# Optimization experiments

Measured on AMD Instinct MI355X. Metric: run time of the kernel, lower is better.

## Reference

```python
import jax, jax.numpy as jnp
import numpy as np

N = 50000      # nodes
E = 600000     # edges (avg degree 12)
F_IN = 64      # raw node features
HID = 128      # hidden_size
HEADS = 8
DH = HID // HEADS  # 16, per-head dim = out_channels
C = 10         # classes
L = 3          # num_gnn_layers


def setup_inputs() -> dict:
    key = jax.random.key(0)
    ks = jax.random.split(key, 12)
    g = lambda k, shape, fan: jax.random.normal(k, shape, jnp.float32) / np.float32(np.sqrt(fan))
    return {
        "x": jax.random.normal(ks[0], (N, F_IN), jnp.float32),
        "edge_index": jax.random.randint(ks[1], (2, E), 0, N, dtype=jnp.int32),
        "distance": jax.random.uniform(ks[2], (E, 1), jnp.float32),
        "Wq": g(ks[3], (L, HID, HID), HID), "bq": jnp.zeros((L, HID), jnp.float32),
        "Wk": g(ks[4], (L, HID, HID), HID), "bk": jnp.zeros((L, HID), jnp.float32),
        "Wv": g(ks[5], (L, HID, HID), HID), "bv": jnp.zeros((L, HID), jnp.float32),
        "We": g(ks[6], (L, 1, HID), 1),
        "Ws": g(ks[7], (L, HID, HID), HID), "bs": jnp.zeros((L, HID), jnp.float32),
        "ln_g": jnp.ones((L, HID), jnp.float32), "ln_b": jnp.zeros((L, HID), jnp.float32),
        "W_before": g(ks[8], (F_IN, HID), F_IN), "b_before": jnp.zeros((HID,), jnp.float32),
        "W_after": g(ks[9], (HID, C), HID), "b_after": jnp.zeros((C,), jnp.float32),
    }


def _layer_norm(h, gamma, beta):
    m = h.mean(-1, keepdims=True)
    v = ((h - m) ** 2).mean(-1, keepdims=True)
    return (h - m) * jax.lax.rsqrt(v + 1e-5) * gamma + beta


def _transformer_conv(h, src, dst, ea, Wq, bq, Wk, bk, Wv, bv, We, Ws, bs):
    # PyG TransformerConv (concat=True, beta=False, root_weight=True), eval mode (no dropout)
    q = (h @ Wq + bq).reshape(-1, HEADS, DH)   # [N,H,D]
    k = (h @ Wk + bk).reshape(-1, HEADS, DH)
    v = (h @ Wv + bv).reshape(-1, HEADS, DH)
    e = (ea @ We).reshape(-1, HEADS, DH)       # [E,H,D] edge embedding (no bias)
    ke = k[src] + e                            # gather keys along edges
    alpha = (q[dst] * ke).sum(-1) / np.float32(np.sqrt(DH))  # [E,H]
    # segment softmax over incoming edges per destination node
    amax = jax.ops.segment_max(alpha, dst, num_segments=N)
    amax = jnp.where(jnp.isfinite(amax), amax, 0.0)
    ex = jnp.exp(alpha - amax[dst])
    den = jax.ops.segment_sum(ex, dst, num_segments=N)
    a = ex / (den[dst] + 1e-16)                # [E,H]
    msg = (v[src] + e) * a[..., None]          # weighted values
    out = jax.ops.segment_sum(msg, dst, num_segments=N).reshape(-1, HEADS * DH)
    return out + h @ Ws + bs                   # root/skip connection


def reference(x, edge_index, distance, Wq, bq, Wk, bk, Wv, bv, We, Ws, bs,
              ln_g, ln_b, W_before, b_before, W_after, b_after):
    src, dst = edge_index[0], edge_index[1]
    h = jax.nn.relu(x @ W_before + b_before)   # fcnn_before
    for i in range(L):
        h = _transformer_conv(h, src, dst, distance,
                              Wq[i], bq[i], Wk[i], bk[i], Wv[i], bv[i],
                              We[i], Ws[i], bs[i])
        if i < L - 1:
            h = jax.nn.relu(_layer_norm(h, ln_g[i], ln_b[i]))
    # fcnn_after
    h = jax.nn.relu(_layer_norm(h, ln_g[L - 1], ln_b[L - 1]))
    h = h @ W_after + b_after
    return jax.nn.log_softmax(h, axis=1)
```

## Files before the change

kernel.cpp:

```cpp
#include <hip/hip_runtime.h>
#include <cstdint>
#include <cstddef>

#define NN 50000
#define NE 600000
#define FIN 64
#define HID 128
#define NCLS 10
#define NLAYER 3

#define QSCALE 0.36067376022224085f

typedef __bf16 bf16x8 __attribute__((ext_vector_type(8)));
typedef float f32x4 __attribute__((ext_vector_type(4)));
typedef float f32x2 __attribute__((ext_vector_type(2)));

__device__ __forceinline__ unsigned short f2bf(float f) {
    unsigned int u = __builtin_bit_cast(unsigned int, f);
    u += 0x7fffu + ((u >> 16) & 1u);
    return (unsigned short)(u >> 16);
}
__device__ __forceinline__ float bf2f(unsigned short s) {
    unsigned int u = ((unsigned int)s) << 16;
    return __builtin_bit_cast(float, u);
}

__global__ __launch_bounds__(256) void k_prep(
    const float* __restrict__ Wq, const float* __restrict__ Wk,
    const float* __restrict__ Wv, const float* __restrict__ Ws,
    const float* __restrict__ Wbe, const float* __restrict__ Waf,
    unsigned short* __restrict__ Wt12,
    unsigned short* __restrict__ Wbt,
    float* __restrict__ Wat,
    const int* __restrict__ edst, int* __restrict__ counts)
{
    int blk = blockIdx.x;
    int tid = threadIdx.x;
    if (blk < 768) {
        int m = blk >> 6;
        int l = m >> 2, which = m & 3;
        const float* src;
        if (which == 0) src = Wq; else if (which == 1) src = Wk;
        else if (which == 2) src = Wv; else src = Ws;
        src += (size_t)l * HID * HID;
        int idx = (blk & 63) * 256 + tid;
        int c = idx >> 7, k = idx & 127;
        Wt12[(size_t)m * 16384 + (size_t)c * 128 + k] = f2bf(src[(size_t)k * 128 + c]);
    } else if (blk < 800) {
        int idx = (blk - 768) * 256 + tid;
        int c = idx >> 6, k = idx & 63;
        Wbt[(size_t)c * 64 + k] = f2bf(Wbe[(size_t)k * 128 + c]);
    } else if (blk < 805) {
        int i = (blk - 800) * 256 + tid;
        if (i < 1280) {
            int c = i >> 7, f = i & 127;
            Wat[i] = Waf[f * 10 + c];
        }
    } else {
        int e = (blk - 805) * 256 + tid;
        if (e < NE) atomicAdd(&counts[edst[e]], 1);
    }
}

__global__ __launch_bounds__(512) void k_scan1(const int* __restrict__ counts,
                                               int* __restrict__ row_ptr,
                                               int* __restrict__ partials, int n) {
    __shared__ int sm[512];
    int tid = threadIdx.x;
    int i = blockIdx.x * 512 + tid;
    int v = (i < n) ? counts[i] : 0;
    sm[tid] = v;
    __syncthreads();
    #pragma unroll
    for (int off = 1; off < 512; off <<= 1) {
        int t = (tid >= off) ? sm[tid - off] : 0;
        __syncthreads();
        sm[tid] += t;
        __syncthreads();
    }
    if (i < n) row_ptr[i] = sm[tid] - v;
    if (tid == 511) partials[blockIdx.x] = sm[511];
}

__global__ __launch_bounds__(128) void k_scan2(int* __restrict__ partials, int nb) {
    __shared__ int sm[128];
    int t = threadIdx.x;
    int v = (t < nb) ? partials[t] : 0;
    sm[t] = v;
    __syncthreads();
    #pragma unroll
    for (int off = 1; off < 128; off <<= 1) {
        int x = (t >= off) ? sm[t - off] : 0;
        __syncthreads();
        sm[t] += x;
        __syncthreads();
    }
    if (t < nb) partials[t] = sm[t] - v;
}

__global__ __launch_bounds__(512) void k_scan3(int* __restrict__ row_ptr,
                                               const int* __restrict__ partials, int n) {
    int i = blockIdx.x * 512 + threadIdx.x;
    if (i < n) row_ptr[i] += partials[blockIdx.x];
}

__global__ __launch_bounds__(256) void k_fill(const int* __restrict__ esrc,
                                              const int* __restrict__ edst,
                                              const float* __restrict__ dist,
                                              int* __restrict__ cursor,
                                              const int* __restrict__ row_ptr,
                                              int2* __restrict__ srcd) {
    int e = blockIdx.x * 256 + threadIdx.x;
    if (e < NE) {
        int d = edst[e];
        int pos = atomicAdd(&cursor[d], 1);
        srcd[row_ptr[d] + pos] = make_int2(esrc[e], __float_as_int(dist[e]));
    }
}

__device__ __forceinline__ void qkvs_store(
    int m, int arow, int colb, f32x4 acc, float4 bb, int nrows,
    unsigned short* __restrict__ qb, unsigned char* __restrict__ kv8,
    unsigned short* __restrict__ hsb)
{
    if (arow >= nrows) return;
    float v0 = acc[0] + bb.x, v1 = acc[1] + bb.y;
    float v2 = acc[2] + bb.z, v3 = acc[3] + bb.w;
    if (m == 0) {
        ushort4 o;
        o.x = f2bf(v0 * QSCALE); o.y = f2bf(v1 * QSCALE);
        o.z = f2bf(v2 * QSCALE); o.w = f2bf(v3 * QSCALE);
        *(ushort4*)(qb + (size_t)arow * 128 + colb) = o;
    } else if (m == 1 || m == 2) {
        unsigned int pk = __builtin_amdgcn_cvt_pk_fp8_f32(v0, v1, 0, false);
        pk = __builtin_amdgcn_cvt_pk_fp8_f32(v2, v3, pk, true);
        *(unsigned int*)(kv8 + (size_t)arow * 256 + (colb >> 2) * 8 + (m == 2 ? 4 : 0)) = pk;
    } else {
        ushort4 o;
        o.x = f2bf(v0); o.y = f2bf(v1); o.z = f2bf(v2); o.w = f2bf(v3);
        *(ushort4*)(hsb + (size_t)arow * 128 + colb) = o;
    }
}

__global__ __launch_bounds__(512) void k_qkvs(
    const unsigned short* __restrict__ Ab, int nrows,
    const unsigned short* __restrict__ Wt,
    const float* __restrict__ bq, const float* __restrict__ bk,
    const float* __restrict__ bv, const float* __restrict__ bs,
    unsigned short* __restrict__ qb,
    unsigned char* __restrict__ kv8,
    unsigned short* __restrict__ hsb)
{
    const int tid = threadIdx.x;
    const int w = tid >> 6, lane = tid & 63;
    const int m = w >> 1, ch = w & 1;
    const float* bias = (m == 0) ? bq : (m == 1) ? bk : (m == 2) ? bv : bs;
    const unsigned short* Wm = Wt + (size_t)m * 16384;
    const int lc = lane & 15, lk = lane >> 4;

    bf16x8 bw[4][4];
    float4 bb[4];
    #pragma unroll
    for (int ct = 0; ct < 4; ++ct) {
        int col = ch * 64 + ct * 16 + lc;
        bb[ct] = *(const float4*)(bias + ch * 64 + ct * 16 + lk * 4);
        #pragma unroll
        for (int kb = 0; kb < 4; ++kb)
            bw[ct][kb] = *(const bf16x8*)(Wm + (size_t)col * 128 + kb * 32 + lk * 8);
    }

    const int r0 = blockIdx.x * 64;
    #pragma unroll
    for (int rt = 0; rt < 4; ++rt) {
        const int arow = r0 + rt * 16 + lc;
        const bool rv = arow < nrows;
        bf16x8 z = {};
        bf16x8 a[4];
        #pragma unroll
        for (int kb = 0; kb < 4; ++kb)
            a[kb] = rv ? *(const bf16x8*)(Ab + (size_t)arow * 128 + kb * 32 + lk * 8) : z;
        #pragma unroll
        for (int ct = 0; ct < 4; ++ct) {
            f32x4 acc = {0.f, 0.f, 0.f, 0.f};
            #pragma unroll
            for (int kb = 0; kb < 4; ++kb)
                acc = __builtin_amdgcn_mfma_f32_16x16x32_bf16(bw[ct][kb], a[kb], acc, 0, 0, 0);
            qkvs_store(m, arow, ch * 64 + ct * 16 + lk * 4, acc, bb[ct], nrows, qb, kv8, hsb);
        }
    }
}

__global__ __launch_bounds__(512) void k_gqkvs(
    const float* __restrict__ x, int nrows,
    const unsigned short* __restrict__ Wbt,
    const float* __restrict__ bbe,
    const unsigned short* __restrict__ Wt,
    const float* __restrict__ bq, const float* __restrict__ bk,
    const float* __restrict__ bv, const float* __restrict__ bs,
    unsigned short* __restrict__ qb,
    unsigned char* __restrict__ kv8,
    unsigned short* __restrict__ hsb)
{
    __shared__ unsigned short hs_s[64 * 136];
    const int tid = threadIdx.x;
    const int w = tid >> 6, lane = tid & 63;
    const int lc = lane & 15, lk = lane >> 4;
    const int r0 = blockIdx.x * 64;

    {
        const int rt0 = w & 3, ch0 = w >> 2;
        const int arl = rt0 * 16 + lc;
        const int arow = r0 + arl;
        const bool rv = arow < nrows;
        bf16x8 a[2];
        #pragma unroll
        for (int kb = 0; kb < 2; ++kb) {
            union { bf16x8 v; unsigned short u[8]; } t;
            #pragma unroll
            for (int q = 0; q < 2; ++q) {
                float4 f = rv ? *(const float4*)(x + (size_t)arow * 64 + kb * 32 + lk * 8 + q * 4)
                              : make_float4(0.f, 0.f, 0.f, 0.f);
                t.u[q * 4 + 0] = f2bf(f.x); t.u[q * 4 + 1] = f2bf(f.y);
                t.u[q * 4 + 2] = f2bf(f.z); t.u[q * 4 + 3] = f2bf(f.w);
            }
            a[kb] = t.v;
        }
        #pragma unroll
        for (int ct = 0; ct < 4; ++ct) {
            const int col = ch0 * 64 + ct * 16 + lc;
            f32x4 acc = {0.f, 0.f, 0.f, 0.f};
            #pragma unroll
            for (int kb = 0; kb < 2; ++kb) {
                bf16x8 bwf = *(const bf16x8*)(Wbt + (size_t)col * 64 + kb * 32 + lk * 8);
                acc = __builtin_amdgcn_mfma_f32_16x16x32_bf16(bwf, a[kb], acc, 0, 0, 0);
            }
            float4 bv_ = *(const float4*)(bbe + ch0 * 64 + ct * 16 + lk * 4);
            ushort4 o;
            o.x = rv ? f2bf(fmaxf(acc[0] + bv_.x, 0.f)) : 0;
            o.y = rv ? f2bf(fmaxf(acc[1] + bv_.y, 0.f)) : 0;
            o.z = rv ? f2bf(fmaxf(acc[2] + bv_.z, 0.f)) : 0;
            o.w = rv ? f2bf(fmaxf(acc[3] + bv_.w, 0.f)) : 0;
            *(ushort4*)(hs_s + arl * 136 + ch0 * 64 + ct * 16 + lk * 4) = o;
        }
    }
    __syncthreads();

    const int m = w >> 1, ch = w & 1;
    const float* bias = (m == 0) ? bq : (m == 1) ? bk : (m == 2) ? bv : bs;
    const unsigned short* Wm = Wt + (size_t)m * 16384;

    bf16x8 bw[4][4];
    float4 bb[4];
    #pragma unroll
    for (int ct = 0; ct < 4; ++ct) {
        int col = ch * 64 + ct * 16 + lc;
        bb[ct] = *(const float4*)(bias + ch * 64 + ct * 16 + lk * 4);
        #pragma unroll
        for (int kb = 0; kb < 4; ++kb)
            bw[ct][kb] = *(const bf16x8*)(Wm + (size_t)col * 128 + kb * 32 + lk * 8);
    }

    #pragma unroll
    for (int rt = 0; rt < 4; ++rt) {
        const int arl = rt * 16 + lc;
        const int arow = r0 + arl;
        bf16x8 a[4];
        #pragma unroll
        for (int kb = 0; kb < 4; ++kb)
            a[kb] = *(const bf16x8*)(hs_s + arl * 136 + kb * 32 + lk * 8);
        #pragma unroll
        for (int ct = 0; ct < 4; ++ct) {
            f32x4 acc = {0.f, 0.f, 0.f, 0.f};
            #pragma unroll
            for (int kb = 0; kb < 4; ++kb)
                acc = __builtin_amdgcn_mfma_f32_16x16x32_bf16(bw[ct][kb], a[kb], acc, 0, 0, 0);
            qkvs_store(m, arow, ch * 64 + ct * 16 + lk * 4, acc, bb[ct], nrows, qb, kv8, hsb);
        }
    }
}

#define FET(Ki, i) {                                                      \
    int e_ = base + 2 * (i) + half;                                       \
    int ec_ = e_ < cmax ? e_ : 0;                                         \
    int sx_ = __shfl(sd0.x, ec_);                                         \
    Ki = *(const uint2*)(kv8 + (size_t)sx_ * 256 + l5 * 8); }

#define CMP(Ki, i) {                                                      \
    int e_ = base + 2 * (i) + half;                                       \
    bool val_ = e_ < cmax;                                                \
    int ec_ = val_ ? e_ : 0;                                              \
    float dd_ = __int_as_float(__shfl(sd0.y, ec_));                       \
    f32x2 k01_ = __builtin_amdgcn_cvt_pk_f32_fp8(Ki.x, false);            \
    f32x2 k23_ = __builtin_amdgcn_cvt_pk_f32_fp8(Ki.x, true);             \
    float p_ = q0 * k01_.x + q1 * k01_.y + q2 * k23_.x + q3 * k23_.y;     \
    p_ += __shfl_xor(p_, 1);                                              \
    p_ += __shfl_xor(p_, 2);                                              \
    p_ = fmaf(dd_, qwe, p_);                                              \
    float w_ = val_ ? exp2f(p_) : 0.f;                                    \
    s += w_;                                                              \
    sd = fmaf(dd_, w_, sd);                                               \
    f32x2 v01_ = __builtin_amdgcn_cvt_pk_f32_fp8(Ki.y, false);            \
    f32x2 v23_ = __builtin_amdgcn_cvt_pk_f32_fp8(Ki.y, true);             \
    va0 = fmaf(v01_.x, w_, va0); va1 = fmaf(v01_.y, w_, va1);             \
    va2 = fmaf(v23_.x, w_, va2); va3 = fmaf(v23_.y, w_, va3); }

template <int LAST>
__global__ __launch_bounds__(256, 6) void k_attn(
    const unsigned short* __restrict__ qb,
    const unsigned short* __restrict__ hsb,
    const unsigned char* __restrict__ kv8,
    const int2* __restrict__ srcd,
    const float* __restrict__ We,
    const int* __restrict__ row_ptr,
    const float* __restrict__ lng,
    const float* __restrict__ lnb,
    unsigned short* __restrict__ hb,
    const float* __restrict__ Wat,
    const float* __restrict__ ba,
    float* __restrict__ out, int nnodes)
{
    const int wid = threadIdx.x >> 6;
    const int lane = threadIdx.x & 63;
    const int n = blockIdx.x * 4 + wid;
    if (n >= nnodes) return;
    const int half = lane >> 5;
    const int l5 = lane & 31;
    const int d0 = l5 * 4;

    const int beg = row_ptr[n];
    const int cnt = row_ptr[n + 1] - beg;

    ushort4 qu = *(const ushort4*)(qb + (size_t)n * 128 + d0);
    const float q0 = bf2f(qu.x), q1 = bf2f(qu.y), q2 = bf2f(qu.z), q3 = bf2f(qu.w);
    const float4 wv = *(const float4*)(We + d0);
    float qwe = q0 * wv.x + q1 * wv.y + q2 * wv.z + q3 * wv.w;
    qwe += __shfl_xor(qwe, 1);
    qwe += __shfl_xor(qwe, 2);

    float s = 0.f, sd = 0.f;
    float va0 = 0.f, va1 = 0.f, va2 = 0.f, va3 = 0.f;

    if (cnt > 0) {
        int2 sd0 = srcd[beg + (lane < cnt ? lane : 0)];
        const int cmax = cnt < 64 ? cnt : 64;
        const int nch = (cmax + 15) >> 4;
        for (int ch = 0; ch < nch; ++ch) {
            const int base = ch << 4;
            uint2 kA, kB, kC, kD, kE, kF, kG, kH;
            FET(kA, 0) FET(kB, 1) FET(kC, 2) FET(kD, 3)
            FET(kE, 4) FET(kF, 5) FET(kG, 6) FET(kH, 7)
            CMP(kA, 0) CMP(kB, 1) CMP(kC, 2) CMP(kD, 3)
            CMP(kE, 4) CMP(kF, 5) CMP(kG, 6) CMP(kH, 7)
        }
        for (int e = 64 + half; e < cnt; e += 2) {
            int2 sde = srcd[beg + e];
            uint2 kr = *(const uint2*)(kv8 + (size_t)sde.x * 256 + l5 * 8);
            float dd_ = __int_as_float(sde.y);
            f32x2 k01_ = __builtin_amdgcn_cvt_pk_f32_fp8(kr.x, false);
            f32x2 k23_ = __builtin_amdgcn_cvt_pk_f32_fp8(kr.x, true);
            float p_ = q0 * k01_.x + q1 * k01_.y + q2 * k23_.x + q3 * k23_.y;
            p_ += __shfl_xor(p_, 1);
            p_ += __shfl_xor(p_, 2);
            p_ = fmaf(dd_, qwe, p_);
            float w_ = exp2f(p_);
            s += w_;
            sd = fmaf(dd_, w_, sd);
            f32x2 v01_ = __builtin_amdgcn_cvt_pk_f32_fp8(kr.y, false);
            f32x2 v23_ = __builtin_amdgcn_cvt_pk_f32_fp8(kr.y, true);
            va0 = fmaf(v01_.x, w_, va0); va1 = fmaf(v01_.y, w_, va1);
            va2 = fmaf(v23_.x, w_, va2); va3 = fmaf(v23_.y, w_, va3);
        }
    }

    s  += __shfl_xor(s, 32);
    sd += __shfl_xor(sd, 32);
    va0 += __shfl_xor(va0, 32);
    va1 += __shfl_xor(va1, 32);
    va2 += __shfl_xor(va2, 32);
    va3 += __shfl_xor(va3, 32);

    const float inv = 1.f / (s + 1e-16f);
    const ushort4 hu = *(const ushort4*)(hsb + (size_t)n * 128 + d0);
    float o0 = fmaf(fmaf(wv.x, sd, va0), inv, bf2f(hu.x));
    float o1 = fmaf(fmaf(wv.y, sd, va1), inv, bf2f(hu.y));
    float o2 = fmaf(fmaf(wv.z, sd, va2), inv, bf2f(hu.z));
    float o3 = fmaf(fmaf(wv.w, sd, va3), inv, bf2f(hu.w));

    float tt = o0 + o1 + o2 + o3;
    #pragma unroll
    for (int msk = 1; msk < 32; msk <<= 1) tt += __shfl_xor(tt, msk);
    const float mean = tt * 0.0078125f;
    const float e0 = o0 - mean, e1 = o1 - mean, e2 = o2 - mean, e3 = o3 - mean;
    float vv2 = e0 * e0 + e1 * e1 + e2 * e2 + e3 * e3;
    #pragma unroll
    for (int msk = 1; msk < 32; msk <<= 1) vv2 += __shfl_xor(vv2, msk);
    const float rstd = rsqrtf(vv2 * 0.0078125f + 1e-5f);
    const float4 g4 = *(const float4*)(lng + d0);
    const float4 b4 = *(const float4*)(lnb + d0);
    const float y0 = fmaxf(fmaf(e0 * rstd, g4.x, b4.x), 0.f);
    const float y1 = fmaxf(fmaf(e1 * rstd, g4.y, b4.y), 0.f);
    const float y2 = fmaxf(fmaf(e2 * rstd, g4.z, b4.z), 0.f);
    const float y3 = fmaxf(fmaf(e3 * rstd, g4.w, b4.w), 0.f);

    if (LAST) {
        float lg[NCLS];
        #pragma unroll
        for (int c = 0; c < NCLS; ++c) {
            float4 wa = *(const float4*)(Wat + c * 128 + d0);
            float p = y0 * wa.x + y1 * wa.y + y2 * wa.z + y3 * wa.w;
            #pragma unroll
            for (int msk = 1; msk < 32; msk <<= 1) p += __shfl_xor(p, msk);
            lg[c] = p + ba[c];
        }
        float mx = lg[0];
        #pragma unroll
        for (int c = 1; c < NCLS; ++c) mx = fmaxf(mx, lg[c]);
        float sum = 0.f;
        #pragma unroll
        for (int c = 0; c < NCLS; ++c) sum += __expf(lg[c] - mx);
        float lse = mx + __logf(sum);
        if (lane == 0) {
            #pragma unroll
            for (int c = 0; c < NCLS; ++c) out[(size_t)n * NCLS + c] = lg[c] - lse;
        }
    } else if (lane < 32) {
        ushort4 o;
        o.x = f2bf(y0); o.y = f2bf(y1); o.z = f2bf(y2); o.w = f2bf(y3);
        *(ushort4*)(hb + (size_t)n * 128 + d0) = o;
    }
}

extern "C" void kernel_launch(void* const* d_in, const int* in_sizes, int n_in,
                              void* d_out, int out_size, void* d_ws, size_t ws_size,
                              hipStream_t stream)
{
    const float* x    = (const float*)d_in[0];
    const int*   ei   = (const int*)d_in[1];
    const float* dist = (const float*)d_in[2];
    const float* Wq   = (const float*)d_in[3];
    const float* bq   = (const float*)d_in[4];
    const float* Wk   = (const float*)d_in[5];
    const float* bk   = (const float*)d_in[6];
    const float* Wv   = (const float*)d_in[7];
    const float* bv   = (const float*)d_in[8];
    const float* We   = (const float*)d_in[9];
    const float* Wsk  = (const float*)d_in[10];
    const float* bs   = (const float*)d_in[11];
    const float* lng  = (const float*)d_in[12];
    const float* lnb  = (const float*)d_in[13];
    const float* Wbe  = (const float*)d_in[14];
    const float* bbe  = (const float*)d_in[15];
    const float* Waf  = (const float*)d_in[16];
    const float* baf  = (const float*)d_in[17];
    float* out = (float*)d_out;
    const int* esrc = ei;
    const int* edst = ei + NE;

    char* ws = (char*)d_ws;
    size_t off = 0;
    unsigned short* qb  = (unsigned short*)(ws + off); off += 12800000;
    unsigned short* hsb = (unsigned short*)(ws + off); off += 12800000;
    unsigned char*  kv8 = (unsigned char*)(ws + off);  off += 12800000;
    unsigned short* hb  = (unsigned short*)(ws + off); off += 12800000;
    unsigned short* Wt12 = (unsigned short*)(ws + off); off += 393216;
    unsigned short* Wbt  = (unsigned short*)(ws + off); off += 16384;
    float* Wat = (float*)(ws + off);   off += 5120;
    int* counts   = (int*)(ws + off);  off += 200192;
    int* cursor   = (int*)(ws + off);  off += 200192;
    int* row_ptr  = (int*)(ws + off);  off += 200192;
    int* partials = (int*)(ws + off);  off += 512;
    int2* srcd    = (int2*)(ws + off); off += (size_t)NE * 8 + 512;

    hipMemsetAsync(counts, 0, 2 * 200192, stream);
    k_prep<<<805 + (NE + 255) / 256, 256, 0, stream>>>(
        Wq, Wk, Wv, Wsk, Wbe, Waf, Wt12, Wbt, Wat, edst, counts);
    int nsb = (NN + 1 + 511) / 512;
    k_scan1<<<nsb, 512, 0, stream>>>(counts, row_ptr, partials, NN + 1);
    k_scan2<<<1, 128, 0, stream>>>(partials, nsb);
    k_scan3<<<nsb, 512, 0, stream>>>(row_ptr, partials, NN + 1);
    k_fill<<<(NE + 255) / 256, 256, 0, stream>>>(esrc, edst, dist, cursor, row_ptr, srcd);

    const int ngb = (NN + 63) / 64;
    const int nab = (NN + 3) / 4;

    for (int l = 0; l < NLAYER; ++l) {
        const unsigned short* wt = Wt12 + (size_t)l * 4 * 16384;
        if (l == 0) {
            k_gqkvs<<<ngb, 512, 0, stream>>>(x, NN, Wbt, bbe, wt,
                bq, bk, bv, bs, qb, kv8, hsb);
        } else {
            k_qkvs<<<ngb, 512, 0, stream>>>(hb, NN, wt,
                bq + l * HID, bk + l * HID, bv + l * HID, bs + l * HID,
                qb, kv8, hsb);
        }
        if (l < NLAYER - 1) {
            k_attn<0><<<nab, 256, 0, stream>>>(qb, hsb, kv8, srcd, We + l * HID,
                row_ptr, lng + l * HID, lnb + l * HID, hb, nullptr, nullptr, nullptr, NN);
        } else {
            k_attn<1><<<nab, 256, 0, stream>>>(qb, hsb, kv8, srcd, We + l * HID,
                row_ptr, lng + l * HID, lnb + l * HID, hb, Wat, baf, out, NN);
        }
    }
}
```

Before: 342.0 us.

## Process five destination nodes per wave with shared edge-window staging

Each wave now handles NPW=5 consecutive destination nodes instead of one. It loads their combined edge list (up to 128 entries) into a per-wave LDS window in one coalesced pass, falling back to global srcd reads for overflow. The q/hs rows for the next node are prefetched while the current node computes, and launch bounds rise to 7 waves per SIMD. This amortizes row_ptr/srcd load latency and launch overhead, at the cost of LDS usage, serialized per-node work within a wave, and possible load imbalance.

```diff
diff --git a/kernel.cpp b/kernel.cpp
--- a/kernel.cpp
+++ b/kernel.cpp
@@ -8,6 +8,7 @@
 #define HID 128
 #define NCLS 10
 #define NLAYER 3
+#define NPW 5
 
 #define QSCALE 0.36067376022224085f
 
@@ -279,33 +280,33 @@
     }
 }
 
-#define FET(Ki, i) {                                                      \
-    int e_ = base + 2 * (i) + half;                                       \
-    int ec_ = e_ < cmax ? e_ : 0;                                         \
-    int sx_ = __shfl(sd0.x, ec_);                                         \
-    Ki = *(const uint2*)(kv8 + (size_t)sx_ * 256 + l5 * 8); }
-
-#define CMP(Ki, i) {                                                      \
-    int e_ = base + 2 * (i) + half;                                       \
-    bool val_ = e_ < cmax;                                                \
-    int ec_ = val_ ? e_ : 0;                                              \
-    float dd_ = __int_as_float(__shfl(sd0.y, ec_));                       \
-    f32x2 k01_ = __builtin_amdgcn_cvt_pk_f32_fp8(Ki.x, false);            \
-    f32x2 k23_ = __builtin_amdgcn_cvt_pk_f32_fp8(Ki.x, true);             \
+#define FET(i) {                                                          \
+    int rel_ = base + 2 * (i) + half;                                     \
+    int rc_ = rel_ < bloc ? rel_ : aloc;                                  \
+    int2 sv_;                                                             \
+    if (rc_ < 128) sv_ = win[rc_];                                        \
+    else           sv_ = srcd[e0 + rc_];                                  \
+    D##i = __int_as_float(sv_.y);                                         \
+    K##i = *(const uint2*)(kv8 + (size_t)sv_.x * 256 + l5 * 8); }
+
+#define CMP(i) {                                                          \
+    bool v_ = (base + 2 * (i) + half) < bloc;                             \
+    f32x2 k01_ = __builtin_amdgcn_cvt_pk_f32_fp8(K##i.x, false);          \
+    f32x2 k23_ = __builtin_amdgcn_cvt_pk_f32_fp8(K##i.x, true);           \
     float p_ = q0 * k01_.x + q1 * k01_.y + q2 * k23_.x + q3 * k23_.y;     \
     p_ += __shfl_xor(p_, 1);                                              \
     p_ += __shfl_xor(p_, 2);                                              \
-    p_ = fmaf(dd_, qwe, p_);                                              \
-    float w_ = val_ ? exp2f(p_) : 0.f;                                    \
+    p_ = fmaf(D##i, qwe, p_);                                             \
+    float w_ = v_ ? exp2f(p_) : 0.f;                                      \
     s += w_;                                                              \
-    sd = fmaf(dd_, w_, sd);                                               \
-    f32x2 v01_ = __builtin_amdgcn_cvt_pk_f32_fp8(Ki.y, false);            \
-    f32x2 v23_ = __builtin_amdgcn_cvt_pk_f32_fp8(Ki.y, true);             \
+    sd = fmaf(D##i, w_, sd);                                              \
+    f32x2 v01_ = __builtin_amdgcn_cvt_pk_f32_fp8(K##i.y, false);          \
+    f32x2 v23_ = __builtin_amdgcn_cvt_pk_f32_fp8(K##i.y, true);           \
     va0 = fmaf(v01_.x, w_, va0); va1 = fmaf(v01_.y, w_, va1);             \
     va2 = fmaf(v23_.x, w_, va2); va3 = fmaf(v23_.y, w_, va3); }
 
 template <int LAST>
-__global__ __launch_bounds__(256, 6) void k_attn(
+__global__ __launch_bounds__(256, 7) void k_attn(
     const unsigned short* __restrict__ qb,
     const unsigned short* __restrict__ hsb,
     const unsigned char* __restrict__ kv8,
@@ -319,114 +320,119 @@
     const float* __restrict__ ba,
     float* __restrict__ out, int nnodes)
 {
+    __shared__ int2 ewin[4][128];
     const int wid = threadIdx.x >> 6;
     const int lane = threadIdx.x & 63;
-    const int n = blockIdx.x * 4 + wid;
-    if (n >= nnodes) return;
+    const int b0 = (blockIdx.x * 4 + wid) * NPW;
+    if (b0 >= nnodes) return;
+    int2* win = ewin[wid];
     const int half = lane >> 5;
     const int l5 = lane & 31;
     const int d0 = l5 * 4;
 
-    const int beg = row_ptr[n];
-    const int cnt = row_ptr[n + 1] - beg;
-
-    ushort4 qu = *(const ushort4*)(qb + (size_t)n * 128 + d0);
-    const float q0 = bf2f(qu.x), q1 = bf2f(qu.y), q2 = bf2f(qu.z), q3 = bf2f(qu.w);
+    const int rpv = row_ptr[b0 + (lane < NPW ? lane : NPW)];
+    const int e0 = __shfl(rpv, 0);
+    const int T = __shfl(rpv, NPW) - e0;
+
+    {
+        int i0 = lane, i1 = 64 + lane;
+        int2 wa = srcd[e0 + (i0 < T ? i0 : 0)];
+        int2 wb = srcd[e0 + (i1 < T ? i1 : 0)];
+        win[i0] = wa;
+        win[i1] = wb;
+    }
+    asm volatile("s_waitcnt lgkmcnt(0)" ::: "memory");
+
     const float4 wv = *(const float4*)(We + d0);
-    float qwe = q0 * wv.x + q1 * wv.y + q2 * wv.z + q3 * wv.w;
-    qwe += __shfl_xor(qwe, 1);
-    qwe += __shfl_xor(qwe, 2);
-
-    float s = 0.f, sd = 0.f;
-    float va0 = 0.f, va1 = 0.f, va2 = 0.f, va3 = 0.f;
-
-    if (cnt > 0) {
-        int2 sd0 = srcd[beg + (lane < cnt ? lane : 0)];
-        const int cmax = cnt < 64 ? cnt : 64;
-        const int nch = (cmax + 15) >> 4;
-        for (int ch = 0; ch < nch; ++ch) {
-            const int base = ch << 4;
-            uint2 kA, kB, kC, kD, kE, kF, kG, kH;
-            FET(kA, 0) FET(kB, 1) FET(kC, 2) FET(kD, 3)
-            FET(kE, 4) FET(kF, 5) FET(kG, 6) FET(kH, 7)
-            CMP(kA, 0) CMP(kB, 1) CMP(kC, 2) CMP(kD, 3)
-            CMP(kE, 4) CMP(kF, 5) CMP(kG, 6) CMP(kH, 7)
-        }
-        for (int e = 64 + half; e < cnt; e += 2) {
-            int2 sde = srcd[beg + e];
-            uint2 kr = *(const uint2*)(kv8 + (size_t)sde.x * 256 + l5 * 8);
-            float dd_ = __int_as_float(sde.y);
-            f32x2 k01_ = __builtin_amdgcn_cvt_pk_f32_fp8(kr.x, false);
-            f32x2 k23_ = __builtin_amdgcn_cvt_pk_f32_fp8(kr.x, true);
-            float p_ = q0 * k01_.x + q1 * k01_.y + q2 * k23_.x + q3 * k23_.y;
-            p_ += __shfl_xor(p_, 1);
-            p_ += __shfl_xor(p_, 2);
-            p_ = fmaf(dd_, qwe, p_);
-            float w_ = exp2f(p_);
-            s += w_;
-            sd = fmaf(dd_, w_, sd);
-            f32x2 v01_ = __builtin_amdgcn_cvt_pk_f32_fp8(kr.y, false);
-            f32x2 v23_ = __builtin_amdgcn_cvt_pk_f32_fp8(kr.y, true);
-            va0 = fmaf(v01_.x, w_, va0); va1 = fmaf(v01_.y, w_, va1);
-            va2 = fmaf(v23_.x, w_, va2); va3 = fmaf(v23_.y, w_, va3);
-        }
-    }
-
-    s  += __shfl_xor(s, 32);
-    sd += __shfl_xor(sd, 32);
-    va0 += __shfl_xor(va0, 32);
-    va1 += __shfl_xor(va1, 32);
-    va2 += __shfl_xor(va2, 32);
-    va3 += __shfl_xor(va3, 32);
-
-    const float inv = 1.f / (s + 1e-16f);
-    const ushort4 hu = *(const ushort4*)(hsb + (size_t)n * 128 + d0);
-    float o0 = fmaf(fmaf(wv.x, sd, va0), inv, bf2f(hu.x));
-    float o1 = fmaf(fmaf(wv.y, sd, va1), inv, bf2f(hu.y));
-    float o2 = fmaf(fmaf(wv.z, sd, va2), inv, bf2f(hu.z));
-    float o3 = fmaf(fmaf(wv.w, sd, va3), inv, bf2f(hu.w));
-
-    float tt = o0 + o1 + o2 + o3;
-    #pragma unroll
-    for (int msk = 1; msk < 32; msk <<= 1) tt += __shfl_xor(tt, msk);
-    const float mean = tt * 0.0078125f;
-    const float e0 = o0 - mean, e1 = o1 - mean, e2 = o2 - mean, e3 = o3 - mean;
-    float vv2 = e0 * e0 + e1 * e1 + e2 * e2 + e3 * e3;
-    #pragma unroll
-    for (int msk = 1; msk < 32; msk <<= 1) vv2 += __shfl_xor(vv2, msk);
-    const float rstd = rsqrtf(vv2 * 0.0078125f + 1e-5f);
-    const float4 g4 = *(const float4*)(lng + d0);
-    const float4 b4 = *(const float4*)(lnb + d0);
-    const float y0 = fmaxf(fmaf(e0 * rstd, g4.x, b4.x), 0.f);
-    const float y1 = fmaxf(fmaf(e1 * rstd, g4.y, b4.y), 0.f);
-    const float y2 = fmaxf(fmaf(e2 * rstd, g4.z, b4.z), 0.f);
-    const float y3 = fmaxf(fmaf(e3 * rstd, g4.w, b4.w), 0.f);
-
-    if (LAST) {
-        float lg[NCLS];
-        #pragma unroll
-        for (int c = 0; c < NCLS; ++c) {
-            float4 wa = *(const float4*)(Wat + c * 128 + d0);
-            float p = y0 * wa.x + y1 * wa.y + y2 * wa.z + y3 * wa.w;
-            #pragma unroll
-            for (int msk = 1; msk < 32; msk <<= 1) p += __shfl_xor(p, msk);
-            lg[c] = p + ba[c];
-        }
-        float mx = lg[0];
-        #pragma unroll
-        for (int c = 1; c < NCLS; ++c) mx = fmaxf(mx, lg[c]);
-        float sum = 0.f;
-        #pragma unroll
-        for (int c = 0; c < NCLS; ++c) sum += __expf(lg[c] - mx);
-        float lse = mx + __logf(sum);
-        if (lane == 0) {
-            #pragma unroll
-            for (int c = 0; c < NCLS; ++c) out[(size_t)n * NCLS + c] = lg[c] - lse;
-        }
-    } else if (lane < 32) {
-        ushort4 o;
-        o.x = f2bf(y0); o.y = f2bf(y1); o.z = f2bf(y2); o.w = f2bf(y3);
-        *(ushort4*)(hb + (size_t)n * 128 + d0) = o;
+
+    ushort4 qcur = *(const ushort4*)(qb + (size_t)b0 * 128 + d0);
+    ushort4 hcur = *(const ushort4*)(hsb + (size_t)b0 * 128 + d0);
+
+    for (int ni = 0; ni < NPW; ++ni) {
+        const int n = b0 + ni;
+        if (n >= nnodes) break;
+        const int aloc = __shfl(rpv, ni) - e0;
+        const int bloc = __shfl(rpv, ni + 1) - e0;
+
+        const float q0 = bf2f(qcur.x), q1 = bf2f(qcur.y);
+        const float q2 = bf2f(qcur.z), q3 = bf2f(qcur.w);
+        float qwe = q0 * wv.x + q1 * wv.y + q2 * wv.z + q3 * wv.w;
+        qwe += __shfl_xor(qwe, 1);
+        qwe += __shfl_xor(qwe, 2);
+
+        ushort4 qnx = qcur, hnx = hcur;
+        if (ni + 1 < NPW && n + 1 < nnodes) {
+            qnx = *(const ushort4*)(qb + (size_t)(n + 1) * 128 + d0);
+            hnx = *(const ushort4*)(hsb + (size_t)(n + 1) * 128 + d0);
+        }
+
+        float s = 0.f, sd = 0.f;
+        float va0 = 0.f, va1 = 0.f, va2 = 0.f, va3 = 0.f;
+        for (int base = aloc; base < bloc; base += 16) {
+            float D0, D1, D2, D3, D4, D5, D6, D7;
+            uint2 K0, K1, K2, K3, K4, K5, K6, K7;
+            FET(0) FET(1) FET(2) FET(3) FET(4) FET(5) FET(6) FET(7)
+            CMP(0) CMP(1) CMP(2) CMP(3) CMP(4) CMP(5) CMP(6) CMP(7)
+        }
+
+        s  += __shfl_xor(s, 32);
+        sd += __shfl_xor(sd, 32);
+        va0 += __shfl_xor(va0, 32);
+        va1 += __shfl_xor(va1, 32);
+        va2 += __shfl_xor(va2, 32);
+        va3 += __shfl_xor(va3, 32);
+
+        const float inv = 1.f / (s + 1e-16f);
+        float o0 = fmaf(fmaf(wv.x, sd, va0), inv, bf2f(hcur.x));
+        float o1 = fmaf(fmaf(wv.y, sd, va1), inv, bf2f(hcur.y));
+        float o2 = fmaf(fmaf(wv.z, sd, va2), inv, bf2f(hcur.z));
+        float o3 = fmaf(fmaf(wv.w, sd, va3), inv, bf2f(hcur.w));
+
+        float tt = o0 + o1 + o2 + o3;
+        #pragma unroll
+        for (int msk = 1; msk < 32; msk <<= 1) tt += __shfl_xor(tt, msk);
+        const float mean = tt * 0.0078125f;
+        const float e0f = o0 - mean, e1f = o1 - mean;
+        const float e2f = o2 - mean, e3f = o3 - mean;
+        float vv2 = e0f * e0f + e1f * e1f + e2f * e2f + e3f * e3f;
+        #pragma unroll
+        for (int msk = 1; msk < 32; msk <<= 1) vv2 += __shfl_xor(vv2, msk);
+        const float rstd = rsqrtf(vv2 * 0.0078125f + 1e-5f);
+        const float4 g4 = *(const float4*)(lng + d0);
+        const float4 b4 = *(const float4*)(lnb + d0);
+        const float y0 = fmaxf(fmaf(e0f * rstd, g4.x, b4.x), 0.f);
+        const float y1 = fmaxf(fmaf(e1f * rstd, g4.y, b4.y), 0.f);
+        const float y2 = fmaxf(fmaf(e2f * rstd, g4.z, b4.z), 0.f);
+        const float y3 = fmaxf(fmaf(e3f * rstd, g4.w, b4.w), 0.f);
+
+        if (LAST) {
+            float lg[NCLS];
+            #pragma unroll
+            for (int c = 0; c < NCLS; ++c) {
+                float4 wa = *(const float4*)(Wat + c * 128 + d0);
+                float p = y0 * wa.x + y1 * wa.y + y2 * wa.z + y3 * wa.w;
+                #pragma unroll
+                for (int msk = 1; msk < 32; msk <<= 1) p += __shfl_xor(p, msk);
+                lg[c] = p + ba[c];
+            }
+            float mx = lg[0];
+            #pragma unroll
+            for (int c = 1; c < NCLS; ++c) mx = fmaxf(mx, lg[c]);
+            float sum = 0.f;
+            #pragma unroll
+            for (int c = 0; c < NCLS; ++c) sum += __expf(lg[c] - mx);
+            float lse = mx + __logf(sum);
+            if (lane == 0) {
+                #pragma unroll
+                for (int c = 0; c < NCLS; ++c) out[(size_t)n * NCLS + c] = lg[c] - lse;
+            }
+        } else if (lane < 32) {
+            ushort4 o;
+            o.x = f2bf(y0); o.y = f2bf(y1); o.z = f2bf(y2); o.w = f2bf(y3);
+            *(ushort4*)(hb + (size_t)n * 128 + d0) = o;
+        }
+        qcur = qnx;
+        hcur = hnx;
     }
 }
 
@@ -469,7 +475,7 @@
     int* cursor   = (int*)(ws + off);  off += 200192;
     int* row_ptr  = (int*)(ws + off);  off += 200192;
     int* partials = (int*)(ws + off);  off += 512;
-    int2* srcd    = (int2*)(ws + off); off += (size_t)NE * 8 + 512;
+    int2* srcd    = (int2*)(ws + off); off += (size_t)NE * 8 + 4096;
 
     hipMemsetAsync(counts, 0, 2 * 200192, stream);
     k_prep<<<805 + (NE + 255) / 256, 256, 0, stream>>>(
@@ -481,7 +487,8 @@
     k_fill<<<(NE + 255) / 256, 256, 0, stream>>>(esrc, edst, dist, cursor, row_ptr, srcd);
 
     const int ngb = (NN + 63) / 64;
-    const int nab = (NN + 3) / 4;
+    const int nwv = (NN + NPW - 1) / NPW;
+    const int nab = (nwv + 3) / 4;
 
     for (int l = 0; l < NLAYER; ++l) {
         const unsigned short* wt = Wt12 + (size_t)l * 4 * 16384;
```

New measurement: 516.9 us. +51.1%, slower.
